# Kernel optimization log

Hardware: AMD Instinct MI355X
Metric: run time of the kernel (lower is better)

The kernel has to match this reference:

```python
import jax, jax.numpy as jnp
import numpy as np

NUM_HEADS = 12


def setup_inputs() -> dict:
    key = jax.random.key(0)
    k1, k2, k3 = jax.random.split(key, 3)
    B, N, C = 2, 2048, 768
    x = jax.random.normal(k1, (B, N, C), dtype=jnp.float32)
    # xavier_uniform-ish scaled weights
    w_qkv = jax.random.normal(k2, (C, 3 * C), dtype=jnp.float32) * (1.0 / np.sqrt(C))
    w_proj = jax.random.normal(k3, (C, C), dtype=jnp.float32) * (1.0 / np.sqrt(C))
    b_proj = jnp.zeros((C,), dtype=jnp.float32)
    return {"x": x, "w_qkv": w_qkv, "w_proj": w_proj, "b_proj": b_proj}


def reference(x, w_qkv, w_proj, b_proj):
    B, N, C = x.shape
    H = NUM_HEADS
    D = C // H
    scale = D ** -0.5
    # [B, N, 3, H, D]
    qkv = (x @ w_qkv).reshape(B, N, 3, H, D)
    q = qkv[:, :, 0].transpose(0, 2, 1, 3)  # [B, H, N, D]
    k = qkv[:, :, 1].transpose(0, 2, 1, 3)
    v = qkv[:, :, 2].transpose(0, 2, 1, 3)
    attn = jnp.einsum("bhnd,bhmd->bhnm", q, k) * scale  # [B, H, N, N]
    attn = jax.nn.softmax(attn, axis=-1)  # attn_drop = 0.0 -> identity
    out = jnp.einsum("bhnm,bhmd->bhnd", attn, v)  # [B, H, N, D]
    out = out.transpose(0, 2, 1, 3).reshape(B, N, C)
    return out @ w_proj + b_proj  # proj_drop = 0.0 -> identity
```

## Files before the change

### kernel.cpp

```cpp
#include <hip/hip_runtime.h>
#include <hip/hip_bf16.h>

typedef __attribute__((ext_vector_type(8))) short short8;
typedef __attribute__((ext_vector_type(4))) float f32x4;
typedef __attribute__((ext_vector_type(4))) int int4v;

#define HD 64
#define NH 12
#define SEQ 2048
#define CDIM 768
#define NT (SEQ / 64)

#define QSCALE 0.180336880f

static __device__ __forceinline__ unsigned short f2bf(float f) {
    __hip_bfloat16 h = __float2bfloat16(f);
    return __builtin_bit_cast(unsigned short, h);
}

static __device__ __forceinline__ unsigned cvtpk_bf16(float a, float b) {
    unsigned r;
    asm("v_cvt_pk_bf16_f32 %0, %1, %2" : "=v"(r) : "v"(a), "v"(b));
    return r;
}

#define GLDS16(gp, lp) __builtin_amdgcn_global_load_lds( \
    (const __attribute__((address_space(1))) void*)(gp), \
    (__attribute__((address_space(3))) void*)(lp), 16, 0, 0)

static __device__ __forceinline__ int kperm_f(int r) {
    const int kt = r >> 4, gg = (r >> 2) & 3, jj = r & 3;
    return 32 * (kt & 1) + 8 * gg + 4 * (kt >> 1) + jj;
}

static __device__ __forceinline__ void transpose_tile(const float* __restrict__ in,
        unsigned short* __restrict__ out, int K, int C, int bx, int by,
        float (*t)[33], int tid) {
    const int k0 = bx * 32, c0 = by * 32;
    const int r = tid >> 3, c4 = (tid & 7) * 4;
    const float4 v = *reinterpret_cast<const float4*>(in + (size_t)(k0 + r) * C + c0 + c4);
    t[r][c4 + 0] = v.x; t[r][c4 + 1] = v.y; t[r][c4 + 2] = v.z; t[r][c4 + 3] = v.w;
    __syncthreads();
    ushort4 o;
    o.x = f2bf(t[c4 + 0][r]); o.y = f2bf(t[c4 + 1][r]);
    o.z = f2bf(t[c4 + 2][r]); o.w = f2bf(t[c4 + 3][r]);
    *reinterpret_cast<ushort4*>(out + (size_t)(c0 + r) * K + k0 + c4) = o;
}

__global__ __launch_bounds__(256) void prep_kernel(
        const float* __restrict__ x, const float* __restrict__ wq, const float* __restrict__ wp,
        unsigned short* __restrict__ xb, unsigned short* __restrict__ wqt, unsigned short* __restrict__ wpt) {
    __shared__ float t[32][33];
    const int blk = blockIdx.x, tid = threadIdx.x;
    if (blk < 1728) {
        transpose_tile(wq, wqt, 768, 2304, blk % 24, blk / 24, t, tid);
    } else if (blk < 2304) {
        const int b2 = blk - 1728;
        transpose_tile(wp, wpt, 768, 768, b2 % 24, b2 / 24, t, tid);
    } else {
        const int b3 = blk - 2304;
        #pragma unroll
        for (int it = 0; it < 4; it++) {
            const int i = (b3 * 4 + it) * 256 + tid;
            const float4 v = reinterpret_cast<const float4*>(x)[i];
            ushort4 o;
            o.x = f2bf(v.x); o.y = f2bf(v.y); o.z = f2bf(v.z); o.w = f2bf(v.w);
            reinterpret_cast<ushort4*>(xb)[i] = o;
        }
    }
}

template<int EPI>
__global__ __launch_bounds__(256, 3) void gemm_kernel(
    const unsigned short* __restrict__ A,
    const unsigned short* __restrict__ Bt,
    const int K, const int N,
    unsigned short* __restrict__ Qo, unsigned short* __restrict__ Ko, unsigned short* __restrict__ Vo,
    float* __restrict__ Cout, const float* __restrict__ bias)
{
    const int tid = threadIdx.x;
    const int wave = tid >> 6, lane = tid & 63;
    const int g = lane >> 4, li = lane & 15;
    const int wr = wave >> 1, wc = wave & 1;
    const int m0 = blockIdx.x * 128, n0 = blockIdx.y * 128;

    __shared__ short As[3][128 * 32];
    __shared__ short Bs[3][128 * 32];

    f32x4 acc[4][4];
    #pragma unroll
    for (int i = 0; i < 4; i++)
        #pragma unroll
        for (int j = 0; j < 4; j++)
            acc[i][j] = (f32x4){0.f, 0.f, 0.f, 0.f};

    const int srow = wave * 16 + (lane >> 2);
    const int scol = (lane & 3) * 8;
    const unsigned short* aSrc = A + (size_t)(m0 + srow) * K + scol;
    const unsigned short* bSrc = Bt + (size_t)(n0 + srow) * K + scol;
    const int d0 = wave * 16 * 32, d1 = (wave * 16 + 64) * 32;
    const size_t rowskip = (size_t)64 * K;

    #define GSTAGE(kk, bb) do { \
        GLDS16(aSrc + (kk) * 32,           &As[bb][d0]); \
        GLDS16(aSrc + (kk) * 32 + rowskip, &As[bb][d1]); \
        GLDS16(bSrc + (kk) * 32,           &Bs[bb][d0]); \
        GLDS16(bSrc + (kk) * 32 + rowskip, &Bs[bb][d1]); \
    } while (0)

    const int nk = K >> 5;
    GSTAGE(0, 0);
    GSTAGE(1, 1);
    asm volatile("s_waitcnt vmcnt(4)\n\ts_barrier" ::: "memory");

    int cur = 0;
    for (int kk = 0; kk < nk; ++kk) {
        const int sbuf = (cur == 0) ? 2 : cur - 1;
        const bool stage = (kk + 2 < nk);
        if (stage) GSTAGE(kk + 2, sbuf);
        const short* Ab = As[cur];
        const short* Bb = Bs[cur];
        short8 af[4], bfr[4];
        #pragma unroll
        for (int mf = 0; mf < 4; mf++)
            af[mf] = *reinterpret_cast<const short8*>(&Ab[(wr * 64 + mf * 16 + li) * 32 + 8 * g]);
        #pragma unroll
        for (int nf = 0; nf < 4; nf++)
            bfr[nf] = *reinterpret_cast<const short8*>(&Bb[(wc * 64 + nf * 16 + li) * 32 + 8 * g]);
        __builtin_amdgcn_s_setprio(1);
        #pragma unroll
        for (int mf = 0; mf < 4; mf++)
            #pragma unroll
            for (int nf = 0; nf < 4; nf++)
                acc[mf][nf] = __builtin_amdgcn_mfma_f32_16x16x32_bf16(af[mf], bfr[nf], acc[mf][nf], 0, 0, 0);
        __builtin_amdgcn_s_setprio(0);
        if (stage) asm volatile("s_waitcnt vmcnt(4)\n\ts_barrier" ::: "memory");
        else       asm volatile("s_waitcnt vmcnt(0)\n\ts_barrier" ::: "memory");
        cur = (cur == 2) ? 0 : cur + 1;
    }
    #undef GSTAGE

    #pragma unroll
    for (int mf = 0; mf < 4; mf++) {
        #pragma unroll
        for (int nf = 0; nf < 4; nf++) {
            #pragma unroll
            for (int j = 0; j < 4; j++) {
                const int r = m0 + wr * 64 + mf * 16 + 4 * g + j;
                const int c = n0 + wc * 64 + nf * 16 + li;
                const float v = acc[mf][nf][j];
                if (EPI == 0) {
                    const int s = c / 768, rem = c % 768;
                    const int hh = rem >> 6, d = rem & 63;
                    const int bb = r >> 11, n = r & (SEQ - 1);
                    if (s == 0)
                        Qo[(((size_t)bb * NH + hh) * SEQ + n) * HD + d] = f2bf(v * QSCALE);
                    else if (s == 1)
                        Ko[(((size_t)bb * NH + hh) * SEQ + n) * HD + d] = f2bf(v);
                    else
                        Vo[(((size_t)bb * NH + hh) * HD + d) * SEQ + n] = f2bf(v);
                } else {
                    Cout[(size_t)r * N + c] = v + bias[c];
                }
            }
        }
    }
}

__global__ __launch_bounds__(256, 3) void attn_kernel(
    const unsigned short* __restrict__ Q,
    const unsigned short* __restrict__ Kg,
    const unsigned short* __restrict__ Vtg,
    unsigned short* __restrict__ O)
{
    const int tid = threadIdx.x;
    const int wave = tid >> 6, lane = tid & 63;
    const int g = lane >> 4, li = lane & 15;
    const int head = blockIdx.y;
    const int b = head / NH, h = head % NH;
    const int q0 = blockIdx.x * 64 + wave * 16;
    const size_t plane = (size_t)head * SEQ * HD;

    __shared__ short Ks[3][64 * 64];
    __shared__ short Vs[3][64 * 64];

    short8 qf0, qf1;
    {
        const unsigned short* qp = Q + plane + (size_t)(q0 + li) * HD + 8 * g;
        qf0 = *reinterpret_cast<const short8*>(qp);
        qf1 = *reinterpret_cast<const short8*>(qp + 32);
    }
    const short8 ones = {0x3F80, 0x3F80, 0x3F80, 0x3F80, 0x3F80, 0x3F80, 0x3F80, 0x3F80};

    const int lr = lane >> 3;
    const int colS = ((lane & 7) ^ lr) * 8;
    const int rA = wave * 16 + lr;
    const int rB = rA + 8;
    const unsigned short* kSrcA = Kg + plane + (size_t)kperm_f(rA) * HD + colS;
    const unsigned short* kSrcB = Kg + plane + (size_t)kperm_f(rB) * HD + colS;
    const unsigned short* vSrcA = Vtg + plane + (size_t)rA * SEQ + colS;
    const unsigned short* vSrcB = Vtg + plane + (size_t)rB * SEQ + colS;
    const int stA = wave * 1024, stB = stA + 512;

    #define STAGE(kv, bb) do { \
        GLDS16(kSrcA + (size_t)(kv) * HD, &Ks[bb][stA]); \
        GLDS16(kSrcB + (size_t)(kv) * HD, &Ks[bb][stB]); \
        GLDS16(vSrcA + (kv),              &Vs[bb][stA]); \
        GLDS16(vSrcB + (kv),              &Vs[bb][stB]); \
    } while (0)

    f32x4 o_acc[4], l_acc;
    #pragma unroll
    for (int nf = 0; nf < 4; nf++) o_acc[nf] = (f32x4){0.f, 0.f, 0.f, 0.f};
    l_acc = (f32x4){0.f, 0.f, 0.f, 0.f};

    const int sl0 = (g ^ (li & 7)) * 8;
    const int sl1 = ((g + 4) ^ (li & 7)) * 8;

    STAGE(0, 0);
    STAGE(64, 1);
    asm volatile("s_waitcnt vmcnt(4)\n\ts_barrier" ::: "memory");

    int cur = 0;
    for (int it = 0; it < NT; ++it) {
        const int sbuf = (cur == 0) ? 2 : cur - 1;
        const bool stage = (it + 2 < NT);
        if (stage) STAGE((it + 2) * 64, sbuf);
        const short* Kb = Ks[cur];
        const short* Vb = Vs[cur];

        f32x4 s_acc[4];
        #pragma unroll
        for (int kt = 0; kt < 4; kt++) s_acc[kt] = (f32x4){0.f, 0.f, 0.f, 0.f};
        __builtin_amdgcn_s_setprio(1);
        #pragma unroll
        for (int kt = 0; kt < 4; kt++) {
            const short8 ka0 = *reinterpret_cast<const short8*>(&Kb[(16 * kt + li) * 64 + sl0]);
            const short8 ka1 = *reinterpret_cast<const short8*>(&Kb[(16 * kt + li) * 64 + sl1]);
            s_acc[kt] = __builtin_amdgcn_mfma_f32_16x16x32_bf16(ka0, qf0, s_acc[kt], 0, 0, 0);
            s_acc[kt] = __builtin_amdgcn_mfma_f32_16x16x32_bf16(ka1, qf1, s_acc[kt], 0, 0, 0);
        }
        __builtin_amdgcn_s_setprio(0);

        float p[4][4];
        #pragma unroll
        for (int kt = 0; kt < 4; kt++)
            #pragma unroll
            for (int j = 0; j < 4; j++)
                p[kt][j] = exp2f(s_acc[kt][j]);

        const int4v i0 = { (int)cvtpk_bf16(p[0][0], p[0][1]), (int)cvtpk_bf16(p[0][2], p[0][3]),
                           (int)cvtpk_bf16(p[2][0], p[2][1]), (int)cvtpk_bf16(p[2][2], p[2][3]) };
        const int4v i1 = { (int)cvtpk_bf16(p[1][0], p[1][1]), (int)cvtpk_bf16(p[1][2], p[1][3]),
                           (int)cvtpk_bf16(p[3][0], p[3][1]), (int)cvtpk_bf16(p[3][2], p[3][3]) };
        const short8 pa0 = __builtin_bit_cast(short8, i0);
        const short8 pa1 = __builtin_bit_cast(short8, i1);

        __builtin_amdgcn_s_setprio(1);
        l_acc = __builtin_amdgcn_mfma_f32_16x16x32_bf16(ones, pa0, l_acc, 0, 0, 0);
        l_acc = __builtin_amdgcn_mfma_f32_16x16x32_bf16(ones, pa1, l_acc, 0, 0, 0);
        #pragma unroll
        for (int nf = 0; nf < 4; nf++) {
            const short8 va0 = *reinterpret_cast<const short8*>(&Vb[(16 * nf + li) * 64 + sl0]);
            const short8 va1 = *reinterpret_cast<const short8*>(&Vb[(16 * nf + li) * 64 + sl1]);
            o_acc[nf] = __builtin_amdgcn_mfma_f32_16x16x32_bf16(va0, pa0, o_acc[nf], 0, 0, 0);
            o_acc[nf] = __builtin_amdgcn_mfma_f32_16x16x32_bf16(va1, pa1, o_acc[nf], 0, 0, 0);
        }
        __builtin_amdgcn_s_setprio(0);

        if (stage) asm volatile("s_waitcnt vmcnt(4)\n\ts_barrier" ::: "memory");
        else       asm volatile("s_waitcnt vmcnt(0)\n\ts_barrier" ::: "memory");
        cur = (cur == 2) ? 0 : cur + 1;
    }
    #undef STAGE

    const float inv = 1.0f / l_acc[0];
    unsigned short* dst = O + ((size_t)b * SEQ + q0 + li) * CDIM + h * HD + 4 * g;
    #pragma unroll
    for (int nf = 0; nf < 4; nf++) {
        ushort4 o;
        o.x = f2bf(o_acc[nf][0] * inv);
        o.y = f2bf(o_acc[nf][1] * inv);
        o.z = f2bf(o_acc[nf][2] * inv);
        o.w = f2bf(o_acc[nf][3] * inv);
        *reinterpret_cast<ushort4*>(dst + 16 * nf) = o;
    }
}

extern "C" void kernel_launch(void* const* d_in, const int* in_sizes, int n_in,
                              void* d_out, int out_size, void* d_ws, size_t ws_size,
                              hipStream_t stream) {
    const float* x      = (const float*)d_in[0];
    const float* w_qkv  = (const float*)d_in[1];
    const float* w_proj = (const float*)d_in[2];
    const float* b_proj = (const float*)d_in[3];
    float* out = (float*)d_out;

    char* p = (char*)d_ws;
    auto take = [&](size_t bytes) { char* r = p; p += (bytes + 255) & ~(size_t)255; return r; };
    unsigned short* xb      = (unsigned short*)take((size_t)4096 * 768 * 2);
    unsigned short* wqkv_t  = (unsigned short*)take((size_t)2304 * 768 * 2);
    unsigned short* wproj_t = (unsigned short*)take((size_t)768 * 768 * 2);
    unsigned short* Qb      = (unsigned short*)take((size_t)24 * 2048 * 64 * 2);
    unsigned short* Kb      = (unsigned short*)take((size_t)24 * 2048 * 64 * 2);
    unsigned short* Vb      = (unsigned short*)take((size_t)24 * 2048 * 64 * 2);
    unsigned short* Ob      = (unsigned short*)take((size_t)4096 * 768 * 2);

    prep_kernel<<<3072, 256, 0, stream>>>(x, w_qkv, w_proj, xb, wqkv_t, wproj_t);
    gemm_kernel<0><<<dim3(32, 18), 256, 0, stream>>>(xb, wqkv_t, 768, 2304, Qb, Kb, Vb, nullptr, nullptr);
    attn_kernel<<<dim3(32, 24), 256, 0, stream>>>(Qb, Kb, Vb, Ob);
    gemm_kernel<1><<<dim3(32, 6), 256, 0, stream>>>(Ob, wproj_t, 768, 768, nullptr, nullptr, nullptr, out, b_proj);
}
```

Before: 108.5 us.

## Software-pipeline attention loop: overlap QK of next tile with softmax-PV of previous

Restructures the attention inner loop so each iteration issues the QK^T MFMAs for the current KV tile and then the exp/PV MFMAs for the previous tile, using two alternating score register sets. K buffering drops from three to two LDS buffers while V keeps three rotating buffers. Prefetch depth falls from two tiles ahead to one, and every iteration now waits on vmcnt(0). The aim is to hide the exp/convert latency behind independent matrix work, at the cost of more live registers and less global-load lookahead.

```diff
diff --git a/kernel.cpp b/kernel.cpp
--- a/kernel.cpp
+++ b/kernel.cpp
@@ -167,6 +167,55 @@
     }
 }
 
+
+static __device__ __forceinline__ void qk_mfma(
+    f32x4 (&s)[4], const short* kb, int sl0, int sl1, int li,
+    const short8 qf0, const short8 qf1)
+{
+    #pragma unroll
+    for (int kt = 0; kt < 4; kt++) s[kt] = (f32x4){0.f, 0.f, 0.f, 0.f};
+    __builtin_amdgcn_s_setprio(1);
+    #pragma unroll
+    for (int kt = 0; kt < 4; kt++) {
+        const short8 ka0 = *reinterpret_cast<const short8*>(&kb[(16 * kt + li) * 64 + sl0]);
+        const short8 ka1 = *reinterpret_cast<const short8*>(&kb[(16 * kt + li) * 64 + sl1]);
+        s[kt] = __builtin_amdgcn_mfma_f32_16x16x32_bf16(ka0, qf0, s[kt], 0, 0, 0);
+        s[kt] = __builtin_amdgcn_mfma_f32_16x16x32_bf16(ka1, qf1, s[kt], 0, 0, 0);
+    }
+    __builtin_amdgcn_s_setprio(0);
+}
+
+static __device__ __forceinline__ void sm_pv(
+    const f32x4 (&s)[4], const short* vb, int sl0, int sl1, int li,
+    const short8 ones, f32x4 (&o_acc)[4], f32x4& l_acc)
+{
+    float p[4][4];
+    #pragma unroll
+    for (int kt = 0; kt < 4; kt++)
+        #pragma unroll
+        for (int j = 0; j < 4; j++)
+            p[kt][j] = exp2f(s[kt][j]);
+
+    const int4v i0 = { (int)cvtpk_bf16(p[0][0], p[0][1]), (int)cvtpk_bf16(p[0][2], p[0][3]),
+                       (int)cvtpk_bf16(p[2][0], p[2][1]), (int)cvtpk_bf16(p[2][2], p[2][3]) };
+    const int4v i1 = { (int)cvtpk_bf16(p[1][0], p[1][1]), (int)cvtpk_bf16(p[1][2], p[1][3]),
+                       (int)cvtpk_bf16(p[3][0], p[3][1]), (int)cvtpk_bf16(p[3][2], p[3][3]) };
+    const short8 pa0 = __builtin_bit_cast(short8, i0);
+    const short8 pa1 = __builtin_bit_cast(short8, i1);
+
+    __builtin_amdgcn_s_setprio(1);
+    l_acc = __builtin_amdgcn_mfma_f32_16x16x32_bf16(ones, pa0, l_acc, 0, 0, 0);
+    l_acc = __builtin_amdgcn_mfma_f32_16x16x32_bf16(ones, pa1, l_acc, 0, 0, 0);
+    #pragma unroll
+    for (int nf = 0; nf < 4; nf++) {
+        const short8 va0 = *reinterpret_cast<const short8*>(&vb[(16 * nf + li) * 64 + sl0]);
+        const short8 va1 = *reinterpret_cast<const short8*>(&vb[(16 * nf + li) * 64 + sl1]);
+        o_acc[nf] = __builtin_amdgcn_mfma_f32_16x16x32_bf16(va0, pa0, o_acc[nf], 0, 0, 0);
+        o_acc[nf] = __builtin_amdgcn_mfma_f32_16x16x32_bf16(va1, pa1, o_acc[nf], 0, 0, 0);
+    }
+    __builtin_amdgcn_s_setprio(0);
+}
+
 __global__ __launch_bounds__(256, 3) void attn_kernel(
     const unsigned short* __restrict__ Q,
     const unsigned short* __restrict__ Kg,
@@ -181,7 +230,7 @@
     const int q0 = blockIdx.x * 64 + wave * 16;
     const size_t plane = (size_t)head * SEQ * HD;
 
-    __shared__ short Ks[3][64 * 64];
+    __shared__ short Ks[2][64 * 64];
     __shared__ short Vs[3][64 * 64];
 
     short8 qf0, qf1;
@@ -202,11 +251,11 @@
     const unsigned short* vSrcB = Vtg + plane + (size_t)rB * SEQ + colS;
     const int stA = wave * 1024, stB = stA + 512;
 
-    #define STAGE(kv, bb) do { \
-        GLDS16(kSrcA + (size_t)(kv) * HD, &Ks[bb][stA]); \
-        GLDS16(kSrcB + (size_t)(kv) * HD, &Ks[bb][stB]); \
-        GLDS16(vSrcA + (kv),              &Vs[bb][stA]); \
-        GLDS16(vSrcB + (kv),              &Vs[bb][stB]); \
+    #define STAGE(kv, kbuf, vdst) do { \
+        GLDS16(kSrcA + (size_t)(kv) * HD, &Ks[kbuf][stA]); \
+        GLDS16(kSrcB + (size_t)(kv) * HD, &Ks[kbuf][stB]); \
+        GLDS16(vSrcA + (kv),              (vdst) + stA); \
+        GLDS16(vSrcB + (kv),              (vdst) + stB); \
     } while (0)
 
     f32x4 o_acc[4], l_acc;
@@ -217,62 +266,31 @@
     const int sl0 = (g ^ (li & 7)) * 8;
     const int sl1 = ((g + 4) ^ (li & 7)) * 8;
 
-    STAGE(0, 0);
-    STAGE(64, 1);
-    asm volatile("s_waitcnt vmcnt(4)\n\ts_barrier" ::: "memory");
-
-    int cur = 0;
-    for (int it = 0; it < NT; ++it) {
-        const int sbuf = (cur == 0) ? 2 : cur - 1;
-        const bool stage = (it + 2 < NT);
-        if (stage) STAGE((it + 2) * 64, sbuf);
-        const short* Kb = Ks[cur];
-        const short* Vb = Vs[cur];
-
-        f32x4 s_acc[4];
-        #pragma unroll
-        for (int kt = 0; kt < 4; kt++) s_acc[kt] = (f32x4){0.f, 0.f, 0.f, 0.f};
-        __builtin_amdgcn_s_setprio(1);
-        #pragma unroll
-        for (int kt = 0; kt < 4; kt++) {
-            const short8 ka0 = *reinterpret_cast<const short8*>(&Kb[(16 * kt + li) * 64 + sl0]);
-            const short8 ka1 = *reinterpret_cast<const short8*>(&Kb[(16 * kt + li) * 64 + sl1]);
-            s_acc[kt] = __builtin_amdgcn_mfma_f32_16x16x32_bf16(ka0, qf0, s_acc[kt], 0, 0, 0);
-            s_acc[kt] = __builtin_amdgcn_mfma_f32_16x16x32_bf16(ka1, qf1, s_acc[kt], 0, 0, 0);
-        }
-        __builtin_amdgcn_s_setprio(0);
-
-        float p[4][4];
-        #pragma unroll
-        for (int kt = 0; kt < 4; kt++)
-            #pragma unroll
-            for (int j = 0; j < 4; j++)
-                p[kt][j] = exp2f(s_acc[kt][j]);
-
-        const int4v i0 = { (int)cvtpk_bf16(p[0][0], p[0][1]), (int)cvtpk_bf16(p[0][2], p[0][3]),
-                           (int)cvtpk_bf16(p[2][0], p[2][1]), (int)cvtpk_bf16(p[2][2], p[2][3]) };
-        const int4v i1 = { (int)cvtpk_bf16(p[1][0], p[1][1]), (int)cvtpk_bf16(p[1][2], p[1][3]),
-                           (int)cvtpk_bf16(p[3][0], p[3][1]), (int)cvtpk_bf16(p[3][2], p[3][3]) };
-        const short8 pa0 = __builtin_bit_cast(short8, i0);
-        const short8 pa1 = __builtin_bit_cast(short8, i1);
-
-        __builtin_amdgcn_s_setprio(1);
-        l_acc = __builtin_amdgcn_mfma_f32_16x16x32_bf16(ones, pa0, l_acc, 0, 0, 0);
-        l_acc = __builtin_amdgcn_mfma_f32_16x16x32_bf16(ones, pa1, l_acc, 0, 0, 0);
-        #pragma unroll
-        for (int nf = 0; nf < 4; nf++) {
-            const short8 va0 = *reinterpret_cast<const short8*>(&Vb[(16 * nf + li) * 64 + sl0]);
-            const short8 va1 = *reinterpret_cast<const short8*>(&Vb[(16 * nf + li) * 64 + sl1]);
-            o_acc[nf] = __builtin_amdgcn_mfma_f32_16x16x32_bf16(va0, pa0, o_acc[nf], 0, 0, 0);
-            o_acc[nf] = __builtin_amdgcn_mfma_f32_16x16x32_bf16(va1, pa1, o_acc[nf], 0, 0, 0);
-        }
-        __builtin_amdgcn_s_setprio(0);
-
-        if (stage) asm volatile("s_waitcnt vmcnt(4)\n\ts_barrier" ::: "memory");
-        else       asm volatile("s_waitcnt vmcnt(0)\n\ts_barrier" ::: "memory");
-        cur = (cur == 2) ? 0 : cur + 1;
-    }
+    short* vbP = &Vs[2][0];
+    short* vbC = &Vs[0][0];
+    short* vbN = &Vs[1][0];
+
+    f32x4 sA[4], sB[4];
+
+    STAGE(0, 0, vbC);
+    asm volatile("s_waitcnt vmcnt(0)\n\ts_barrier" ::: "memory");
+
+    #define ITER(IT, SC, SP, DOP) do { \
+        if ((IT) + 1 < NT) STAGE(((IT) + 1) * 64, ((IT) + 1) & 1, vbN); \
+        qk_mfma(SC, &Ks[(IT) & 1][0], sl0, sl1, li, qf0, qf1); \
+        if (DOP) sm_pv(SP, vbP, sl0, sl1, li, ones, o_acc, l_acc); \
+        asm volatile("s_waitcnt vmcnt(0)\n\ts_barrier" ::: "memory"); \
+        { short* t_ = vbP; vbP = vbC; vbC = vbN; vbN = t_; } \
+    } while (0)
+
+    for (int pr = 0; pr < NT / 2; ++pr) {
+        ITER(pr * 2,     sA, sB, pr > 0);
+        ITER(pr * 2 + 1, sB, sA, true);
+    }
+    #undef ITER
     #undef STAGE
+
+    sm_pv(sB, vbP, sl0, sl1, li, ones, o_acc, l_acc);
 
     const float inv = 1.0f / l_acc[0];
     unsigned short* dst = O + ((size_t)b * SEQ + q0 + li) * CDIM + h * HD + 4 * g;
```

New measurement: 106.6 us. No clear change (-1.8%).
